# Performance work log

Measured on AMD Instinct MI355X. Metric: run time of the kernel, lower is better.

The kernel has to match this reference:

```python
import jax, jax.numpy as jnp
import numpy as np


def _wn(v, g):
    # weight norm over input axis: w[:, j] = g[j] * v[:, j] / ||v[:, j]||
    norm = jnp.sqrt(jnp.sum(v * v, axis=0, keepdims=True))
    return v * (g[None, :] / norm)


def setup_inputs() -> dict:
    key = jax.random.key(0)
    ks = jax.random.split(key, 6)
    M, K1, H, OUT = 65536, 512, 1024, 512
    x = jax.random.normal(ks[0], (M, K1), dtype=jnp.float32)
    v1 = jax.random.normal(ks[1], (K1, H), dtype=jnp.float32) * 0.05
    v2 = jax.random.normal(ks[2], (H, H), dtype=jnp.float32) * 0.05
    v3 = jax.random.normal(ks[3], (H, H), dtype=jnp.float32) * 0.05
    v4 = jax.random.normal(ks[4], (H, H), dtype=jnp.float32) * 0.05
    v5 = jax.random.normal(ks[5], (H, OUT), dtype=jnp.float32) * 0.05
    g1 = jnp.ones((H,), jnp.float32)
    g2 = jnp.ones((H,), jnp.float32)
    g3 = jnp.ones((H,), jnp.float32)
    g4 = jnp.ones((H,), jnp.float32)
    g5 = jnp.ones((OUT,), jnp.float32)
    return {"x": x, "v1": v1, "g1": g1, "v2": v2, "g2": g2,
            "v3": v3, "g3": g3, "v4": v4, "g4": g4, "v5": v5, "g5": g5}


def reference(x, v1, g1, v2, g2, v3, g3, v4, g4, v5, g5):
    w1 = _wn(v1, g1)
    w2 = _wn(v2, g2)
    w3 = _wn(v3, g3)
    w4 = _wn(v4, g4)
    w5 = _wn(v5, g5)
    h1 = jax.nn.softplus(x @ w1)    # [M, H]
    h2 = jax.nn.softplus(h1 @ w2)
    h3 = jax.nn.softplus(h2 @ w3)
    h4 = jax.nn.softplus(h3 @ w4)
    out = h4 @ w5                   # final layer linear
    return out
```

## Files before the change

kernel.cpp:

```cpp
#include <hip/hip_runtime.h>
#include <hip/hip_bf16.h>
#include <cstdint>

typedef unsigned short u16;
typedef __attribute__((ext_vector_type(8))) _Float16 f16x8;
typedef __attribute__((ext_vector_type(4))) float f32x4;
typedef __attribute__((ext_vector_type(8))) unsigned short u16x8;

typedef const __attribute__((address_space(1))) void* gas1p;
typedef __attribute__((address_space(3))) void* las3p;
typedef const __attribute__((address_space(3))) u16* lc16p;

__device__ __forceinline__ void gld_lds16(const void* g, void* l) {
    __builtin_amdgcn_global_load_lds((gas1p)g, (las3p)l, 16, 0, 0);
}

template<int OFF>
__device__ __forceinline__ f16x8 dsr128o(const u16* p) {
    f16x8 r;
    asm volatile("ds_read_b128 %0, %1 offset:%2" : "=v"(r) : "v"((lc16p)p), "i"(OFF));
    return r;
}

__device__ __forceinline__ u16 f2h(float f) {
    _Float16 h = (_Float16)f;
    return __builtin_bit_cast(u16, h);
}

__global__ void cvt_x_kernel(const float4* __restrict__ x, u16* __restrict__ xb) {
    size_t i = (size_t)blockIdx.x * blockDim.x + threadIdx.x;
    float4 a = x[2 * i];
    float4 b = x[2 * i + 1];
    u16x8 o;
    o[0] = f2h(a.x); o[1] = f2h(a.y); o[2] = f2h(a.z); o[3] = f2h(a.w);
    o[4] = f2h(b.x); o[5] = f2h(b.y); o[6] = f2h(b.z); o[7] = f2h(b.w);
    *(u16x8*)&xb[i * 8] = o;
}

struct WnDesc {
    const float* v; const float* g; u16* wT; float* partial;
    int K; int N; int blk0;
};
struct WnPack { WnDesc d[5]; int nlayer; };

__global__ void wn_partial_all(WnPack p) {
    int b = blockIdx.x;
    int l = 0;
    while (l + 1 < p.nlayer && b >= p.d[l + 1].blk0) l++;
    const WnDesc& d = p.d[l];
    int lb = b - d.blk0;
    int nbx = d.N >> 6;
    int bx = lb % nbx, seg = lb / nbx;

    int lane = threadIdx.x & 63;
    int tr = threadIdx.x >> 6;
    int n = bx * 64 + lane;
    int kseg = d.K >> 3;
    int kbeg = seg * kseg;
    float s = 0.f;
    for (int k = kbeg + tr; k < kbeg + kseg; k += 4) {
        float x = d.v[(size_t)k * d.N + n];
        s += x * x;
    }
    __shared__ float red[4][64];
    red[tr][lane] = s;
    __syncthreads();
    if (tr == 0)
        d.partial[seg * d.N + n] = red[0][lane] + red[1][lane] + red[2][lane] + red[3][lane];
}

__global__ void wn_write_all(WnPack p) {
    int b = blockIdx.x;
    int l = 0;
    while (l + 1 < p.nlayer && b >= p.d[l + 1].blk0) l++;
    const WnDesc& d = p.d[l];
    int lb = b - d.blk0;
    int nbx = d.N >> 6;
    int bx = lb % nbx, seg = lb / nbx;

    int lane = threadIdx.x & 63;
    int tr = threadIdx.x >> 6;
    int n = bx * 64 + lane;
    float s = 0.f;
#pragma unroll
    for (int i = 0; i < 8; i++) s += d.partial[i * d.N + n];
    float sc = d.g[n] / sqrtf(s);

    int kseg = d.K >> 3;
    int kbeg = seg * kseg;
    for (int k = kbeg + tr; k < kbeg + kseg; k += 4)
        d.wT[(size_t)n * d.K + k] = f2h(d.v[(size_t)k * d.N + n] * sc);
}

template<int N, int K, bool ACT, bool OUTF32>
__global__ __launch_bounds__(512, 2) void gemm_bl2(
    const u16* __restrict__ A, const u16* __restrict__ Bt,
    u16* __restrict__ Ch, float* __restrict__ Cf)
{
    constexpr int M = 65536;
    constexpr int NT = K / 64;
    constexpr int NTN = N / 256;
    constexpr int NWG = (M / 256) * NTN;

    __shared__ u16 sA[2][256 * 64];

    const int bid = blockIdx.x;
    const int wk = (bid & 7) * (NWG >> 3) + (bid >> 3);
    const int tm = wk / NTN, tn = wk % NTN;
    const long m0 = (long)tm * 256;
    const int n0 = tn * 256;

    const int tid = threadIdx.x;
    const int lane = tid & 63;
    const int wid = tid >> 6;
    const int wm = (wid >> 2) * 128;
    const int wn = (wid & 3) * 64;

    const int r8 = tid >> 3;
    const int gcol = ((tid & 7) ^ (r8 & 7)) * 8;
    const u16* Abase = A + (m0 + r8) * (size_t)K + gcol;
    const int dst8 = tid * 8;
    auto stA = [&](int buf, int t) {
        gld_lds16(Abase + (size_t)t * 64, &sA[buf][dst8]);
        gld_lds16(Abase + (size_t)128 * K + (size_t)t * 64, &sA[buf][2 * 4096 + dst8]);
        gld_lds16(Abase + (size_t)64 * K + (size_t)t * 64, &sA[buf][1 * 4096 + dst8]);
        gld_lds16(Abase + (size_t)192 * K + (size_t)t * 64, &sA[buf][3 * 4096 + dst8]);
    };

    const int rbase = lane & 15;
    const int co0 = ((lane >> 4) ^ (lane & 7)) * 8;
    const int arow0 = (wm + rbase) * 64 + co0;

    const int bn = n0 + wn + (lane & 15);
    const int bk = (lane >> 4) * 8;
    auto ldBg = [&](f16x8 (&dst)[2][2], int qn, int t) {
#pragma unroll
        for (int j2 = 0; j2 < 2; j2++)
#pragma unroll
            for (int kk = 0; kk < 2; kk++)
                dst[j2][kk] = *(const f16x8*)&Bt[
                    (size_t)(bn + qn * 32 + j2 * 16) * K + t * 64 + kk * 32 + bk];
    };

    f32x4 acc[8][4] = {};
    f16x8 rA0[4][2], rA1[4][2], B0[2][2], B1[2][2];

    auto mmq = [&](f16x8 (&ra)[4][2], f16x8 (&rb)[2][2], int qm, int qn) {
        __builtin_amdgcn_s_setprio(1);
#pragma unroll
        for (int kk = 0; kk < 2; kk++)
#pragma unroll
            for (int i = 0; i < 4; i++)
#pragma unroll
                for (int j2 = 0; j2 < 2; j2++)
                    acc[qm * 4 + i][qn * 2 + j2] = __builtin_amdgcn_mfma_f32_16x16x32_f16(
                        ra[i][kk], rb[j2][kk], acc[qm * 4 + i][qn * 2 + j2], 0, 0, 0);
        __builtin_amdgcn_s_setprio(0);
    };
    auto BAR = [&]() { __builtin_amdgcn_s_barrier(); };
#define LGKM(n) { asm volatile("s_waitcnt lgkmcnt(" #n ")"); __builtin_amdgcn_sched_barrier(0); }
#define VMC(n)  { asm volatile("s_waitcnt vmcnt(" #n ")");  __builtin_amdgcn_sched_barrier(0); }

    stA(0, 0);
    ldBg(B0, 0, 0);
    ldBg(B1, 1, 0);
    VMC(8);
    BAR();

    for (int t = 0; t < NT; t++) {
        const int cur = t & 1, nxt = cur ^ 1;
        const bool more = (t + 1 < NT);

        const u16* pA0 = &sA[cur][arow0];
        const u16* pA1 = &sA[cur][arow0 ^ 32];
#pragma unroll
        for (int i = 0; i < 4; i++) {
            if (i == 0) { rA0[0][0] = dsr128o<0>(pA0);     rA0[0][1] = dsr128o<0>(pA1); }
            if (i == 1) { rA0[1][0] = dsr128o<2048>(pA0);  rA0[1][1] = dsr128o<2048>(pA1); }
            if (i == 2) { rA0[2][0] = dsr128o<4096>(pA0);  rA0[2][1] = dsr128o<4096>(pA1); }
            if (i == 3) { rA0[3][0] = dsr128o<6144>(pA0);  rA0[3][1] = dsr128o<6144>(pA1); }
        }
#pragma unroll
        for (int i = 0; i < 4; i++) {
            if (i == 0) { rA1[0][0] = dsr128o<8192>(pA0);  rA1[0][1] = dsr128o<8192>(pA1); }
            if (i == 1) { rA1[1][0] = dsr128o<10240>(pA0); rA1[1][1] = dsr128o<10240>(pA1); }
            if (i == 2) { rA1[2][0] = dsr128o<12288>(pA0); rA1[2][1] = dsr128o<12288>(pA1); }
            if (i == 3) { rA1[3][0] = dsr128o<14336>(pA0); rA1[3][1] = dsr128o<14336>(pA1); }
        }
        if (more) stA(nxt, t + 1);

        LGKM(8);
        mmq(rA0, B0, 0, 0);
        mmq(rA0, B1, 0, 1);
        LGKM(0);
        mmq(rA1, B0, 1, 0);
        if (more) ldBg(B0, 0, t + 1);
        mmq(rA1, B1, 1, 1);
        if (more) {
            ldBg(B1, 1, t + 1);
            VMC(8);
            BAR();
        }
    }
#undef LGKM
#undef VMC

    const long crow0 = m0 + wm + ((lane >> 4) << 2);
    const int ccol0 = n0 + wn + (lane & 15);
#pragma unroll
    for (int fi = 0; fi < 8; fi++) {
#pragma unroll
        for (int r = 0; r < 4; r++) {
            const size_t rowoff = (size_t)(crow0 + fi * 16 + r) * N;
#pragma unroll
            for (int fj = 0; fj < 4; fj++) {
                float v = acc[fi][fj][r];
                if (ACT) v = fmaxf(v, 0.f) + __logf(1.f + __expf(-fabsf(v)));
                if (OUTF32) Cf[rowoff + ccol0 + fj * 16] = v;
                else        Ch[rowoff + ccol0 + fj * 16] = f2h(v);
            }
        }
    }
}

extern "C" void kernel_launch(void* const* d_in, const int* in_sizes, int n_in,
                              void* d_out, int out_size, void* d_ws, size_t ws_size,
                              hipStream_t stream) {
    const float* x  = (const float*)d_in[0];
    const float* v1 = (const float*)d_in[1];
    const float* g1 = (const float*)d_in[2];
    const float* v2 = (const float*)d_in[3];
    const float* g2 = (const float*)d_in[4];
    const float* v3 = (const float*)d_in[5];
    const float* g3 = (const float*)d_in[6];
    const float* v4 = (const float*)d_in[7];
    const float* g4 = (const float*)d_in[8];
    const float* v5 = (const float*)d_in[9];
    const float* g5 = (const float*)d_in[10];
    float* out = (float*)d_out;

    const int M = 65536;
    char* ws = (char*)d_ws;
    u16* bufA = (u16*)(ws);
    u16* bufB = (u16*)(ws + 0x8000000ULL);
    u16* w1T  = (u16*)(ws + 0x10000000ULL);
    u16* w2T  = w1T + 1024 * 512;
    u16* w3T  = w2T + 1024 * 1024;
    u16* w4T  = w3T + 1024 * 1024;
    u16* w5T  = w4T + 1024 * 1024;
    float* part = (float*)(ws + 0x10800000ULL);

    cvt_x_kernel<<<(M * 512) / (256 * 8), 256, 0, stream>>>((const float4*)x, bufB);

    WnPack pk;
    int cum = 0;
    auto mk = [&](int i, const float* v, const float* g, u16* wT, int K, int N) {
        pk.d[i] = WnDesc{v, g, wT, part + i * 8 * 1024, K, N, cum};
        cum += (N / 64) * 8;
    };
    mk(0, v1, g1, w1T, 512, 1024);
    mk(1, v2, g2, w2T, 1024, 1024);
    mk(2, v3, g3, w3T, 1024, 1024);
    mk(3, v4, g4, w4T, 1024, 1024);
    mk(4, v5, g5, w5T, 1024, 512);
    pk.nlayer = 5;

    wn_partial_all<<<cum, 256, 0, stream>>>(pk);
    wn_write_all<<<cum, 256, 0, stream>>>(pk);

    gemm_bl2<1024, 512,  true,  false><<<1024, 512, 0, stream>>>(bufB, w1T, bufA, nullptr);
    gemm_bl2<1024, 1024, true,  false><<<1024, 512, 0, stream>>>(bufA, w2T, bufB, nullptr);
    gemm_bl2<1024, 1024, true,  false><<<1024, 512, 0, stream>>>(bufB, w3T, bufA, nullptr);
    gemm_bl2<1024, 1024, true,  false><<<1024, 512, 0, stream>>>(bufA, w4T, bufB, nullptr);
    gemm_bl2<512,  1024, false, true ><<<512,  512, 0, stream>>>(bufB, w5T, nullptr, out);

    (void)in_sizes; (void)n_in; (void)out_size; (void)ws_size;
}
```

Before: 873.8 us.

## Restructure GEMM to 128x256 tiles with LDS-staged B and K=32 steps

Replaces the 256x256 tile GEMM, where B fragments came straight from global memory into registers, with a 128x256 tile that stages both A and B through double-buffered LDS using direct global-to-LDS loads with a rotated swizzle. K-step shrinks from 64 to 32, accumulators drop from 8x4 to 4x4 per wave, and launch bounds go to 4 blocks per CU, all aimed at higher occupancy and lower register pressure. The cost is less reuse per tile, more barriers and full vmcnt/lgkmcnt(0) waits each iteration, and a simpler schedule with less overlap of loads and MFMA work.

```diff
diff --git a/kernel.cpp b/kernel.cpp
--- a/kernel.cpp
+++ b/kernel.cpp
@@ -93,122 +93,91 @@
 }
 
 template<int N, int K, bool ACT, bool OUTF32>
-__global__ __launch_bounds__(512, 2) void gemm_bl2(
+__global__ __launch_bounds__(512, 4) void gemm_mb(
     const u16* __restrict__ A, const u16* __restrict__ Bt,
     u16* __restrict__ Ch, float* __restrict__ Cf)
 {
     constexpr int M = 65536;
-    constexpr int NT = K / 64;
+    constexpr int NT = K / 32;
     constexpr int NTN = N / 256;
-    constexpr int NWG = (M / 256) * NTN;
-
-    __shared__ u16 sA[2][256 * 64];
+    constexpr int NWG = (M / 128) * NTN;
+
+    __shared__ u16 sA[2][128 * 32];
+    __shared__ u16 sB[2][256 * 32];
 
     const int bid = blockIdx.x;
     const int wk = (bid & 7) * (NWG >> 3) + (bid >> 3);
     const int tm = wk / NTN, tn = wk % NTN;
-    const long m0 = (long)tm * 256;
+    const long m0 = (long)tm * 128;
     const int n0 = tn * 256;
 
     const int tid = threadIdx.x;
     const int lane = tid & 63;
     const int wid = tid >> 6;
-    const int wm = (wid >> 2) * 128;
+    const int wm = (wid >> 2) * 64;
     const int wn = (wid & 3) * 64;
 
-    const int r8 = tid >> 3;
-    const int gcol = ((tid & 7) ^ (r8 & 7)) * 8;
-    const u16* Abase = A + (m0 + r8) * (size_t)K + gcol;
+    const int r4 = tid >> 2;
+    const int sG = ((tid & 3) - (r4 & 3)) & 3;
+    const u16* Ab  = A  + (m0 + r4) * (size_t)K + sG * 8;
+    const u16* Bb  = Bt + (size_t)(n0 + r4) * K + sG * 8;
+    const u16* Bb2 = Bt + (size_t)(n0 + 128 + r4) * K + sG * 8;
     const int dst8 = tid * 8;
-    auto stA = [&](int buf, int t) {
-        gld_lds16(Abase + (size_t)t * 64, &sA[buf][dst8]);
-        gld_lds16(Abase + (size_t)128 * K + (size_t)t * 64, &sA[buf][2 * 4096 + dst8]);
-        gld_lds16(Abase + (size_t)64 * K + (size_t)t * 64, &sA[buf][1 * 4096 + dst8]);
-        gld_lds16(Abase + (size_t)192 * K + (size_t)t * 64, &sA[buf][3 * 4096 + dst8]);
+
+    auto stage = [&](int buf, int t) {
+        gld_lds16(Ab + (size_t)t * 32, &sA[buf][dst8]);
+        gld_lds16(Bb + (size_t)t * 32, &sB[buf][dst8]);
+        gld_lds16(Bb2 + (size_t)t * 32, &sB[buf][4096 + dst8]);
     };
 
-    const int rbase = lane & 15;
-    const int co0 = ((lane >> 4) ^ (lane & 7)) * 8;
-    const int arow0 = (wm + rbase) * 64 + co0;
-
-    const int bn = n0 + wn + (lane & 15);
-    const int bk = (lane >> 4) * 8;
-    auto ldBg = [&](f16x8 (&dst)[2][2], int qn, int t) {
-#pragma unroll
-        for (int j2 = 0; j2 < 2; j2++)
-#pragma unroll
-            for (int kk = 0; kk < 2; kk++)
-                dst[j2][kk] = *(const f16x8*)&Bt[
-                    (size_t)(bn + qn * 32 + j2 * 16) * K + t * 64 + kk * 32 + bk];
-    };
-
-    f32x4 acc[8][4] = {};
-    f16x8 rA0[4][2], rA1[4][2], B0[2][2], B1[2][2];
-
-    auto mmq = [&](f16x8 (&ra)[4][2], f16x8 (&rb)[2][2], int qm, int qn) {
-        __builtin_amdgcn_s_setprio(1);
-#pragma unroll
-        for (int kk = 0; kk < 2; kk++)
-#pragma unroll
-            for (int i = 0; i < 4; i++)
-#pragma unroll
-                for (int j2 = 0; j2 < 2; j2++)
-                    acc[qm * 4 + i][qn * 2 + j2] = __builtin_amdgcn_mfma_f32_16x16x32_f16(
-                        ra[i][kk], rb[j2][kk], acc[qm * 4 + i][qn * 2 + j2], 0, 0, 0);
-        __builtin_amdgcn_s_setprio(0);
-    };
+    const int lrow = lane & 15;
+    const int lq = ((lane >> 4) + (lane & 3)) & 3;
+    const int aoff = (wm + lrow) * 32 + lq * 8;
+    const int boff = (wn + lrow) * 32 + lq * 8;
+
+    f32x4 acc[4][4] = {};
+    f16x8 a[4], b[4];
+
     auto BAR = [&]() { __builtin_amdgcn_s_barrier(); };
-#define LGKM(n) { asm volatile("s_waitcnt lgkmcnt(" #n ")"); __builtin_amdgcn_sched_barrier(0); }
-#define VMC(n)  { asm volatile("s_waitcnt vmcnt(" #n ")");  __builtin_amdgcn_sched_barrier(0); }
-
-    stA(0, 0);
-    ldBg(B0, 0, 0);
-    ldBg(B1, 1, 0);
-    VMC(8);
+#define LGKM0 { asm volatile("s_waitcnt lgkmcnt(0)"); __builtin_amdgcn_sched_barrier(0); }
+#define VMC0  { asm volatile("s_waitcnt vmcnt(0)");  __builtin_amdgcn_sched_barrier(0); }
+
+    stage(0, 0);
+    VMC0;
     BAR();
 
     for (int t = 0; t < NT; t++) {
         const int cur = t & 1, nxt = cur ^ 1;
-        const bool more = (t + 1 < NT);
-
-        const u16* pA0 = &sA[cur][arow0];
-        const u16* pA1 = &sA[cur][arow0 ^ 32];
-#pragma unroll
-        for (int i = 0; i < 4; i++) {
-            if (i == 0) { rA0[0][0] = dsr128o<0>(pA0);     rA0[0][1] = dsr128o<0>(pA1); }
-            if (i == 1) { rA0[1][0] = dsr128o<2048>(pA0);  rA0[1][1] = dsr128o<2048>(pA1); }
-            if (i == 2) { rA0[2][0] = dsr128o<4096>(pA0);  rA0[2][1] = dsr128o<4096>(pA1); }
-            if (i == 3) { rA0[3][0] = dsr128o<6144>(pA0);  rA0[3][1] = dsr128o<6144>(pA1); }
-        }
-#pragma unroll
-        for (int i = 0; i < 4; i++) {
-            if (i == 0) { rA1[0][0] = dsr128o<8192>(pA0);  rA1[0][1] = dsr128o<8192>(pA1); }
-            if (i == 1) { rA1[1][0] = dsr128o<10240>(pA0); rA1[1][1] = dsr128o<10240>(pA1); }
-            if (i == 2) { rA1[2][0] = dsr128o<12288>(pA0); rA1[2][1] = dsr128o<12288>(pA1); }
-            if (i == 3) { rA1[3][0] = dsr128o<14336>(pA0); rA1[3][1] = dsr128o<14336>(pA1); }
-        }
-        if (more) stA(nxt, t + 1);
-
-        LGKM(8);
-        mmq(rA0, B0, 0, 0);
-        mmq(rA0, B1, 0, 1);
-        LGKM(0);
-        mmq(rA1, B0, 1, 0);
-        if (more) ldBg(B0, 0, t + 1);
-        mmq(rA1, B1, 1, 1);
-        if (more) {
-            ldBg(B1, 1, t + 1);
-            VMC(8);
+        if (t + 1 < NT) stage(nxt, t + 1);
+
+        const u16* pA = &sA[cur][aoff];
+        const u16* pB = &sB[cur][boff];
+        a[0] = dsr128o<0>(pA);    a[1] = dsr128o<1024>(pA);
+        a[2] = dsr128o<2048>(pA); a[3] = dsr128o<3072>(pA);
+        b[0] = dsr128o<0>(pB);    b[1] = dsr128o<1024>(pB);
+        b[2] = dsr128o<2048>(pB); b[3] = dsr128o<3072>(pB);
+        LGKM0;
+
+        __builtin_amdgcn_s_setprio(1);
+#pragma unroll
+        for (int i = 0; i < 4; i++)
+#pragma unroll
+            for (int j = 0; j < 4; j++)
+                acc[i][j] = __builtin_amdgcn_mfma_f32_16x16x32_f16(a[i], b[j], acc[i][j], 0, 0, 0);
+        __builtin_amdgcn_s_setprio(0);
+
+        if (t + 1 < NT) {
+            VMC0;
             BAR();
         }
     }
-#undef LGKM
-#undef VMC
+#undef LGKM0
+#undef VMC0
 
     const long crow0 = m0 + wm + ((lane >> 4) << 2);
     const int ccol0 = n0 + wn + (lane & 15);
 #pragma unroll
-    for (int fi = 0; fi < 8; fi++) {
+    for (int fi = 0; fi < 4; fi++) {
 #pragma unroll
         for (int r = 0; r < 4; r++) {
             const size_t rowoff = (size_t)(crow0 + fi * 16 + r) * N;
@@ -268,11 +237,11 @@
     wn_partial_all<<<cum, 256, 0, stream>>>(pk);
     wn_write_all<<<cum, 256, 0, stream>>>(pk);
 
-    gemm_bl2<1024, 512,  true,  false><<<1024, 512, 0, stream>>>(bufB, w1T, bufA, nullptr);
-    gemm_bl2<1024, 1024, true,  false><<<1024, 512, 0, stream>>>(bufA, w2T, bufB, nullptr);
-    gemm_bl2<1024, 1024, true,  false><<<1024, 512, 0, stream>>>(bufB, w3T, bufA, nullptr);
-    gemm_bl2<1024, 1024, true,  false><<<1024, 512, 0, stream>>>(bufA, w4T, bufB, nullptr);
-    gemm_bl2<512,  1024, false, true ><<<512,  512, 0, stream>>>(bufB, w5T, nullptr, out);
+    gemm_mb<1024, 512,  true,  false><<<2048, 512, 0, stream>>>(bufB, w1T, bufA, nullptr);
+    gemm_mb<1024, 1024, true,  false><<<2048, 512, 0, stream>>>(bufA, w2T, bufB, nullptr);
+    gemm_mb<1024, 1024, true,  false><<<2048, 512, 0, stream>>>(bufB, w3T, bufA, nullptr);
+    gemm_mb<1024, 1024, true,  false><<<2048, 512, 0, stream>>>(bufA, w4T, bufB, nullptr);
+    gemm_mb<512,  1024, false, true ><<<1024, 512, 0, stream>>>(bufB, w5T, nullptr, out);
 
     (void)in_sizes; (void)n_in; (void)out_size; (void)ws_size;
 }
```

Measured after the change: 755.3 us. -13.6%, faster.

## Warp-specialize GEMM with producer waves staging A and B tiles into LDS

Applied to the files above, without the earlier changes.

Splits each 640-thread GEMM block into 8 compute waves and 2 producer waves. The producer waves stream both A and B tiles into double-buffered LDS with global_load_lds, and the compute waves now read B from LDS instead of loading it per-wave from global memory. The aim is to take global-load latency and issue off the MFMA waves and to share B across the waves. In exchange LDS use doubles to 128KB per block and launch_bounds drops the 2-blocks-per-CU hint, which likely limits occupancy to one block per CU. Each iteration now waits on a full-drain vmcnt(0) plus a block-wide barrier.

```diff
diff --git a/kernel.cpp b/kernel.cpp
--- a/kernel.cpp
+++ b/kernel.cpp
@@ -15,10 +15,9 @@
     __builtin_amdgcn_global_load_lds((gas1p)g, (las3p)l, 16, 0, 0);
 }
 
-template<int OFF>
-__device__ __forceinline__ f16x8 dsr128o(const u16* p) {
+__device__ __forceinline__ f16x8 dsr128(const u16* p) {
     f16x8 r;
-    asm volatile("ds_read_b128 %0, %1 offset:%2" : "=v"(r) : "v"((lc16p)p), "i"(OFF));
+    asm volatile("ds_read_b128 %0, %1" : "=v"(r) : "v"((lc16p)p));
     return r;
 }
 
@@ -93,7 +92,7 @@
 }
 
 template<int N, int K, bool ACT, bool OUTF32>
-__global__ __launch_bounds__(512, 2) void gemm_bl2(
+__global__ __launch_bounds__(640) void gemm_pc(
     const u16* __restrict__ A, const u16* __restrict__ Bt,
     u16* __restrict__ Ch, float* __restrict__ Cf)
 {
@@ -103,6 +102,7 @@
     constexpr int NWG = (M / 256) * NTN;
 
     __shared__ u16 sA[2][256 * 64];
+    __shared__ u16 sB[2][2 * 128 * 64];
 
     const int bid = blockIdx.x;
     const int wk = (bid & 7) * (NWG >> 3) + (bid >> 3);
@@ -113,39 +113,75 @@
     const int tid = threadIdx.x;
     const int lane = tid & 63;
     const int wid = tid >> 6;
+
+#define VMC0 { asm volatile("s_waitcnt vmcnt(0)"); __builtin_amdgcn_sched_barrier(0); }
+#define LGKM(n) { asm volatile("s_waitcnt lgkmcnt(" #n ")"); __builtin_amdgcn_sched_barrier(0); }
+
+    if (wid >= 8) {
+        const int pw = wid - 8;
+        const int lr = lane >> 3;
+        const int gc = ((lane & 7) ^ lr) * 8;
+        const u16* srcA = A + (m0 + lr) * (size_t)K + gc;
+        const u16* srcB = Bt + (size_t)(n0 + lr) * K + gc;
+        const int BROFF[4] = {0, 128, 32, 160};
+
+        auto stageT = [&](int buf, int t) {
+            if (pw == 0) {
+#pragma unroll
+                for (int c = 0; c < 4; c++)
+#pragma unroll
+                    for (int j = 0; j < 8; j++)
+                        gld_lds16(srcA + (size_t)(c * 64 + j * 8) * K + (size_t)t * 64,
+                                  &sA[buf][c * 4096 + j * 512 + lane * 8]);
+            } else {
+#pragma unroll
+                for (int c = 0; c < 4; c++)
+#pragma unroll
+                    for (int j = 0; j < 8; j++)
+                        gld_lds16(srcB + (size_t)(BROFF[c] + (j >= 4 ? 64 : 0) + (j & 3) * 8) * K
+                                       + (size_t)t * 64,
+                                  &sB[buf][c * 4096 + j * 512 + lane * 8]);
+            }
+        };
+
+        stageT(0, 0);
+        VMC0;
+        __builtin_amdgcn_s_barrier();
+        for (int t = 0; t < NT; t++) {
+            if (t + 1 < NT) stageT((t + 1) & 1, t + 1);
+            VMC0;
+            __builtin_amdgcn_s_barrier();
+        }
+        return;
+    }
+
     const int wm = (wid >> 2) * 128;
     const int wn = (wid & 3) * 64;
-
-    const int r8 = tid >> 3;
-    const int gcol = ((tid & 7) ^ (r8 & 7)) * 8;
-    const u16* Abase = A + (m0 + r8) * (size_t)K + gcol;
-    const int dst8 = tid * 8;
-    auto stA = [&](int buf, int t) {
-        gld_lds16(Abase + (size_t)t * 64, &sA[buf][dst8]);
-        gld_lds16(Abase + (size_t)128 * K + (size_t)t * 64, &sA[buf][2 * 4096 + dst8]);
-        gld_lds16(Abase + (size_t)64 * K + (size_t)t * 64, &sA[buf][1 * 4096 + dst8]);
-        gld_lds16(Abase + (size_t)192 * K + (size_t)t * 64, &sA[buf][3 * 4096 + dst8]);
-    };
-
     const int rbase = lane & 15;
     const int co0 = ((lane >> 4) ^ (lane & 7)) * 8;
     const int arow0 = (wm + rbase) * 64 + co0;
-
-    const int bn = n0 + wn + (lane & 15);
-    const int bk = (lane >> 4) * 8;
-    auto ldBg = [&](f16x8 (&dst)[2][2], int qn, int t) {
-#pragma unroll
-        for (int j2 = 0; j2 < 2; j2++)
-#pragma unroll
-            for (int kk = 0; kk < 2; kk++)
-                dst[j2][kk] = *(const f16x8*)&Bt[
-                    (size_t)(bn + qn * 32 + j2 * 16) * K + t * 64 + kk * 32 + bk];
-    };
+    const int brow0 = ((wn >> 6) * 32 + rbase) * 64 + co0;
 
     f32x4 acc[8][4] = {};
-    f16x8 rA0[4][2], rA1[4][2], B0[2][2], B1[2][2];
-
-    auto mmq = [&](f16x8 (&ra)[4][2], f16x8 (&rb)[2][2], int qm, int qn) {
+    f16x8 rA0[4][2], rA1[4][2], rB0[2][2], rB1[2][2];
+
+    auto dsrA = [&](f16x8 (&r)[4][2], int buf, int qm) {
+#pragma unroll
+        for (int i = 0; i < 4; i++) {
+            int base = arow0 + (qm * 64 + i * 16) * 64;
+            r[i][0] = dsr128(&sA[buf][base]);
+            r[i][1] = dsr128(&sA[buf][base ^ 32]);
+        }
+    };
+    auto dsrB = [&](f16x8 (&r)[2][2], int buf, int qn) {
+#pragma unroll
+        for (int j2 = 0; j2 < 2; j2++) {
+            int base = brow0 + qn * 8192 + j2 * 1024;
+            r[j2][0] = dsr128(&sB[buf][base]);
+            r[j2][1] = dsr128(&sB[buf][base ^ 32]);
+        }
+    };
+    auto mm = [&](f16x8 (&ra)[4][2], f16x8 (&rb)[2][2], int qm, int qn) {
         __builtin_amdgcn_s_setprio(1);
 #pragma unroll
         for (int kk = 0; kk < 2; kk++)
@@ -157,53 +193,25 @@
                         ra[i][kk], rb[j2][kk], acc[qm * 4 + i][qn * 2 + j2], 0, 0, 0);
         __builtin_amdgcn_s_setprio(0);
     };
-    auto BAR = [&]() { __builtin_amdgcn_s_barrier(); };
-#define LGKM(n) { asm volatile("s_waitcnt lgkmcnt(" #n ")"); __builtin_amdgcn_sched_barrier(0); }
-#define VMC(n)  { asm volatile("s_waitcnt vmcnt(" #n ")");  __builtin_amdgcn_sched_barrier(0); }
-
-    stA(0, 0);
-    ldBg(B0, 0, 0);
-    ldBg(B1, 1, 0);
-    VMC(8);
-    BAR();
-
+
+    __builtin_amdgcn_s_barrier();
     for (int t = 0; t < NT; t++) {
-        const int cur = t & 1, nxt = cur ^ 1;
-        const bool more = (t + 1 < NT);
-
-        const u16* pA0 = &sA[cur][arow0];
-        const u16* pA1 = &sA[cur][arow0 ^ 32];
-#pragma unroll
-        for (int i = 0; i < 4; i++) {
-            if (i == 0) { rA0[0][0] = dsr128o<0>(pA0);     rA0[0][1] = dsr128o<0>(pA1); }
-            if (i == 1) { rA0[1][0] = dsr128o<2048>(pA0);  rA0[1][1] = dsr128o<2048>(pA1); }
-            if (i == 2) { rA0[2][0] = dsr128o<4096>(pA0);  rA0[2][1] = dsr128o<4096>(pA1); }
-            if (i == 3) { rA0[3][0] = dsr128o<6144>(pA0);  rA0[3][1] = dsr128o<6144>(pA1); }
-        }
-#pragma unroll
-        for (int i = 0; i < 4; i++) {
-            if (i == 0) { rA1[0][0] = dsr128o<8192>(pA0);  rA1[0][1] = dsr128o<8192>(pA1); }
-            if (i == 1) { rA1[1][0] = dsr128o<10240>(pA0); rA1[1][1] = dsr128o<10240>(pA1); }
-            if (i == 2) { rA1[2][0] = dsr128o<12288>(pA0); rA1[2][1] = dsr128o<12288>(pA1); }
-            if (i == 3) { rA1[3][0] = dsr128o<14336>(pA0); rA1[3][1] = dsr128o<14336>(pA1); }
-        }
-        if (more) stA(nxt, t + 1);
-
+        const int cur = t & 1;
+        dsrA(rA0, cur, 0);
+        dsrB(rB0, cur, 0);
+        dsrB(rB1, cur, 1);
+        dsrA(rA1, cur, 1);
+        LGKM(12);
+        mm(rA0, rB0, 0, 0);
         LGKM(8);
-        mmq(rA0, B0, 0, 0);
-        mmq(rA0, B1, 0, 1);
+        mm(rA0, rB1, 0, 1);
         LGKM(0);
-        mmq(rA1, B0, 1, 0);
-        if (more) ldBg(B0, 0, t + 1);
-        mmq(rA1, B1, 1, 1);
-        if (more) {
-            ldBg(B1, 1, t + 1);
-            VMC(8);
-            BAR();
-        }
-    }
+        mm(rA1, rB0, 1, 0);
+        mm(rA1, rB1, 1, 1);
+        __builtin_amdgcn_s_barrier();
+    }
+#undef VMC0
 #undef LGKM
-#undef VMC
 
     const long crow0 = m0 + wm + ((lane >> 4) << 2);
     const int ccol0 = n0 + wn + (lane & 15);
@@ -268,11 +276,11 @@
     wn_partial_all<<<cum, 256, 0, stream>>>(pk);
     wn_write_all<<<cum, 256, 0, stream>>>(pk);
 
-    gemm_bl2<1024, 512,  true,  false><<<1024, 512, 0, stream>>>(bufB, w1T, bufA, nullptr);
-    gemm_bl2<1024, 1024, true,  false><<<1024, 512, 0, stream>>>(bufA, w2T, bufB, nullptr);
-    gemm_bl2<1024, 1024, true,  false><<<1024, 512, 0, stream>>>(bufB, w3T, bufA, nullptr);
-    gemm_bl2<1024, 1024, true,  false><<<1024, 512, 0, stream>>>(bufA, w4T, bufB, nullptr);
-    gemm_bl2<512,  1024, false, true ><<<512,  512, 0, stream>>>(bufB, w5T, nullptr, out);
+    gemm_pc<1024, 512,  true,  false><<<1024, 640, 0, stream>>>(bufB, w1T, bufA, nullptr);
+    gemm_pc<1024, 1024, true,  false><<<1024, 640, 0, stream>>>(bufA, w2T, bufB, nullptr);
+    gemm_pc<1024, 1024, true,  false><<<1024, 640, 0, stream>>>(bufB, w3T, bufA, nullptr);
+    gemm_pc<1024, 1024, true,  false><<<1024, 640, 0, stream>>>(bufA, w4T, bufB, nullptr);
+    gemm_pc<512,  1024, false, true ><<<512,  640, 0, stream>>>(bufB, w5T, nullptr, out);
 
     (void)in_sizes; (void)n_in; (void)out_size; (void)ws_size;
 }
```

Result: slower. 3.201 ms (+266.3%).
